# Kernel tuning notes

Measured on AMD Instinct MI355X. Metric: run time of the kernel, lower is better.

Reference implementation:

```python
import jax, jax.numpy as jnp
import numpy as np

B, S, H, I = 4, 2048, 4096, 11008

def setup_inputs() -> dict:
    key = jax.random.key(0)
    k0, k1, k2, k3 = jax.random.split(key, 4)
    scale = 0.02  # typical init scale for stability
    return {
        "x": jax.random.normal(k0, (B, S, H), dtype=jnp.float32),
        "w_gate": jax.random.normal(k1, (I, H), dtype=jnp.float32) * scale,
        "w_up": jax.random.normal(k2, (I, H), dtype=jnp.float32) * scale,
        "w_down": jax.random.normal(k3, (H, I), dtype=jnp.float32) * scale,
    }

def reference(x, w_gate, w_up, w_down):
    # gate = x @ w_gate^T, up = x @ w_up^T  (torch F.linear convention)
    gate = jnp.einsum("bsh,ih->bsi", x, w_gate)
    up = jnp.einsum("bsh,ih->bsi", x, w_up)
    inter = jax.nn.silu(gate) * up  # SwiGLU
    return jnp.einsum("bsi,hi->bsh", inter, w_down)
```

## Files before the change

### kernel.cpp

```cpp
#include <hip/hip_runtime.h>
#include <hip/hip_bf16.h>
#include <stdint.h>

static constexpr int Hd = 4096;
static constexpr int Id = 11008;
static constexpr int Md = 8192;

using short8 = __attribute__((ext_vector_type(8))) short;
using f32x4  = __attribute__((ext_vector_type(4))) float;

__device__ __forceinline__ unsigned short f2bf(float x) {
    union { float f; unsigned u; } v; v.f = x;
    unsigned r = v.u + 0x7FFF + ((v.u >> 16) & 1);
    return (unsigned short)(r >> 16);
}

typedef const __attribute__((address_space(1))) unsigned int* as1_u32p;
typedef __attribute__((address_space(3))) unsigned int* as3_u32p;

__device__ __forceinline__ void gload16(const unsigned short* g, unsigned short* l) {
    __builtin_amdgcn_global_load_lds((as1_u32p)(const void*)g, (as3_u32p)(void*)l, 16, 0, 0);
}

#define AOFF(r, c) ((((r) * 8) + ((c) ^ ((r) & 7))) * 8)

#define LGKM0() do { asm volatile("s_waitcnt lgkmcnt(0)" ::: "memory"); \
                     __builtin_amdgcn_sched_barrier(0); } while (0)
#define LGKMC8() do { asm volatile("s_waitcnt lgkmcnt(8)" ::: "memory"); } while (0)
#define VMCNT(n) do { asm volatile("s_waitcnt vmcnt(" #n ")" ::: "memory"); \
                      __builtin_amdgcn_sched_barrier(0); } while (0)
#define BARRIER() do { asm volatile("" ::: "memory"); __builtin_amdgcn_s_barrier(); \
                       asm volatile("" ::: "memory"); } while (0)

__global__ __launch_bounds__(256) void k_cvt4(
    const float* __restrict__ s0, unsigned short* __restrict__ d0, int n0,
    const float* __restrict__ s1, unsigned short* __restrict__ d1, int n1,
    const float* __restrict__ s2, unsigned short* __restrict__ d2, int n2,
    const float* __restrict__ s3, unsigned short* __restrict__ d3, int n3)
{
    const int total = n0 + n1 + n2 + n3;
    int i = blockIdx.x * blockDim.x + threadIdx.x;
    const int stride = gridDim.x * blockDim.x;
    for (; i < total; i += stride) {
        const float* s; unsigned short* d; int j = i;
        if (j < n0) { s = s0; d = d0; }
        else { j -= n0;
            if (j < n1) { s = s1; d = d1; }
            else { j -= n1;
                if (j < n2) { s = s2; d = d2; }
                else { j -= n2; s = s3; d = d3; }
            }
        }
        f32x4 a = *(const f32x4*)(s + (size_t)j * 8);
        f32x4 b = *(const f32x4*)(s + (size_t)j * 8 + 4);
        short8 v;
        v[0] = (short)f2bf(a[0]); v[1] = (short)f2bf(a[1]);
        v[2] = (short)f2bf(a[2]); v[3] = (short)f2bf(a[3]);
        v[4] = (short)f2bf(b[0]); v[5] = (short)f2bf(b[1]);
        v[6] = (short)f2bf(b[2]); v[7] = (short)f2bf(b[3]);
        *reinterpret_cast<short8*>(d + (size_t)j * 8) = v;
    }
}

template<int D>
__device__ __forceinline__ void ug_body(
    unsigned short (&As)[2][2][8192], unsigned short (&Gs)[2][8192], unsigned short (&Us)[2][8192],
    const unsigned short* pA0, const unsigned short* pA1,
    const unsigned short* pG0, const unsigned short* pG1,
    const unsigned short* pU0, const unsigned short* pU1,
    int stA, int stGU, bool pfA, bool pfGU,
    int wm, int wn, int r16, int kg, int wave,
    f32x4 (&accg)[8][2], f32x4 (&accu)[8][2])
{
    constexpr size_t hK = (size_t)128 * Hd;
    short8 af[4][2], gf[2][2], uf[2][2];

    if (pfA) {
        gload16(pA0 + stA, &As[D ^ 1][0][wave * 512]);
        gload16(pA1 + stA, &As[D ^ 1][0][4096 + wave * 512]);
    }
    #pragma unroll
    for (int mi = 0; mi < 4; ++mi)
        #pragma unroll
        for (int kk = 0; kk < 2; ++kk)
            af[mi][kk] = *(const short8*)&As[D][wm][AOFF(mi * 16 + r16, kk * 4 + kg)];
    #pragma unroll
    for (int ni = 0; ni < 2; ++ni)
        #pragma unroll
        for (int kk = 0; kk < 2; ++kk)
            gf[ni][kk] = *(const short8*)&Gs[D][AOFF(wn * 32 + ni * 16 + r16, kk * 4 + kg)];
    LGKMC8();
    BARRIER();
    LGKM0();
    __builtin_amdgcn_s_setprio(1);
    #pragma unroll
    for (int mi = 0; mi < 4; ++mi)
        #pragma unroll
        for (int ni = 0; ni < 2; ++ni)
            #pragma unroll
            for (int kk = 0; kk < 2; ++kk)
                accg[mi][ni] = __builtin_amdgcn_mfma_f32_16x16x32_bf16(af[mi][kk], gf[ni][kk], accg[mi][ni], 0, 0, 0);
    __builtin_amdgcn_s_setprio(0);
    BARRIER();

    if (pfA) {
        gload16(pA0 + hK + stA, &As[D ^ 1][1][wave * 512]);
        gload16(pA1 + hK + stA, &As[D ^ 1][1][4096 + wave * 512]);
    }
    #pragma unroll
    for (int ni = 0; ni < 2; ++ni)
        #pragma unroll
        for (int kk = 0; kk < 2; ++kk)
            uf[ni][kk] = *(const short8*)&Us[D][AOFF(wn * 32 + ni * 16 + r16, kk * 4 + kg)];
    BARRIER();
    LGKM0();
    __builtin_amdgcn_s_setprio(1);
    #pragma unroll
    for (int mi = 0; mi < 4; ++mi)
        #pragma unroll
        for (int ni = 0; ni < 2; ++ni)
            #pragma unroll
            for (int kk = 0; kk < 2; ++kk)
                accu[mi][ni] = __builtin_amdgcn_mfma_f32_16x16x32_bf16(af[mi][kk], uf[ni][kk], accu[mi][ni], 0, 0, 0);
    __builtin_amdgcn_s_setprio(0);
    BARRIER();

    if (pfGU) {
        gload16(pG0 + stGU, &Gs[D][wave * 512]);
        gload16(pG1 + stGU, &Gs[D][4096 + wave * 512]);
    }
    #pragma unroll
    for (int mi = 0; mi < 4; ++mi)
        #pragma unroll
        for (int kk = 0; kk < 2; ++kk)
            af[mi][kk] = *(const short8*)&As[D][wm][AOFF((mi + 4) * 16 + r16, kk * 4 + kg)];
    BARRIER();
    LGKM0();
    __builtin_amdgcn_s_setprio(1);
    #pragma unroll
    for (int mi = 0; mi < 4; ++mi)
        #pragma unroll
        for (int ni = 0; ni < 2; ++ni)
            #pragma unroll
            for (int kk = 0; kk < 2; ++kk)
                accg[mi + 4][ni] = __builtin_amdgcn_mfma_f32_16x16x32_bf16(af[mi][kk], gf[ni][kk], accg[mi + 4][ni], 0, 0, 0);
    __builtin_amdgcn_s_setprio(0);
    BARRIER();

    if (pfGU) {
        gload16(pU0 + stGU, &Us[D][wave * 512]);
        gload16(pU1 + stGU, &Us[D][4096 + wave * 512]);
    }
    __builtin_amdgcn_s_setprio(1);
    #pragma unroll
    for (int mi = 0; mi < 4; ++mi)
        #pragma unroll
        for (int ni = 0; ni < 2; ++ni)
            #pragma unroll
            for (int kk = 0; kk < 2; ++kk)
                accu[mi + 4][ni] = __builtin_amdgcn_mfma_f32_16x16x32_bf16(af[mi][kk], uf[ni][kk], accu[mi + 4][ni], 0, 0, 0);
    __builtin_amdgcn_s_setprio(0);
    if (pfGU) { VMCNT(4); }
    else      { VMCNT(0); }
    BARRIER();
}

__global__ __launch_bounds__(512, 2) void k_upgate(
    const unsigned short* __restrict__ A,
    const unsigned short* __restrict__ G,
    const unsigned short* __restrict__ U,
    unsigned short* __restrict__ inter)
{
    __shared__ unsigned short As[2][2][8192];
    __shared__ unsigned short Gs[2][8192];
    __shared__ unsigned short Us[2][8192];

    const int tid  = threadIdx.x;
    const int wave = tid >> 6;
    const int lane = tid & 63;
    const int wm   = wave >> 2;
    const int wn   = wave & 3;
    const int r16  = lane & 15;
    const int kg   = lane >> 4;

    const int nwg = gridDim.x;
    const int bid = blockIdx.x;
    const int swz = (bid & 7) * (nwg >> 3) + (bid >> 3);
    const int grp = swz / 688;
    const int rem = swz % 688;
    const int m0  = (grp * 8 + (rem & 7)) * 256;
    const int n0  = (rem >> 3) * 128;

    const int i0 = tid,       r0 = i0 >> 3;
    const int i1 = 512 + tid, r1 = i1 >> 3;
    const int cc0 = (i0 & 7) ^ (r0 & 7);
    const int cc1 = (i1 & 7) ^ (r1 & 7);
    constexpr size_t hK = (size_t)128 * Hd;

    const unsigned short* pA0 = A + (size_t)(m0 + r0) * Hd + cc0 * 8;
    const unsigned short* pA1 = A + (size_t)(m0 + r1) * Hd + cc1 * 8;
    const unsigned short* pG0 = G + (size_t)(n0 + r0) * Hd + cc0 * 8;
    const unsigned short* pG1 = G + (size_t)(n0 + r1) * Hd + cc1 * 8;
    const unsigned short* pU0 = U + (size_t)(n0 + r0) * Hd + cc0 * 8;
    const unsigned short* pU1 = U + (size_t)(n0 + r1) * Hd + cc1 * 8;

    f32x4 accg[8][2] = {};
    f32x4 accu[8][2] = {};

    constexpr int NT = Hd >> 6;

    gload16(pA0,      &As[0][0][wave * 512]);
    gload16(pA1,      &As[0][0][4096 + wave * 512]);
    gload16(pA0 + hK, &As[0][1][wave * 512]);
    gload16(pA1 + hK, &As[0][1][4096 + wave * 512]);
    gload16(pG0,      &Gs[0][wave * 512]);
    gload16(pG1,      &Gs[0][4096 + wave * 512]);
    gload16(pU0,      &Us[0][wave * 512]);
    gload16(pU1,      &Us[0][4096 + wave * 512]);
    gload16(pG0 + 64, &Gs[1][wave * 512]);
    gload16(pG1 + 64, &Gs[1][4096 + wave * 512]);
    gload16(pU0 + 64, &Us[1][wave * 512]);
    gload16(pU1 + 64, &Us[1][4096 + wave * 512]);
    VMCNT(4);
    BARRIER();

    for (int kt = 0; kt < NT; kt += 2) {
        ug_body<0>(As, Gs, Us, pA0, pA1, pG0, pG1, pU0, pU1,
                   64, 128, true, (kt + 2) < NT, wm, wn, r16, kg, wave, accg, accu);
        ug_body<1>(As, Gs, Us, pA0, pA1, pG0, pG1, pU0, pU1,
                   128, 192, (kt + 2) < NT, (kt + 3) < NT, wm, wn, r16, kg, wave, accg, accu);
        pA0 += 128; pA1 += 128; pG0 += 128; pG1 += 128; pU0 += 128; pU1 += 128;
    }

    #pragma unroll
    for (int mi = 0; mi < 8; ++mi)
        #pragma unroll
        for (int ni = 0; ni < 2; ++ni) {
            const int row = m0 + wm * 128 + mi * 16 + kg * 4;
            const int col = n0 + wn * 32 + ni * 16 + r16;
            f32x4 g = accg[mi][ni], u = accu[mi][ni];
            #pragma unroll
            for (int rr = 0; rr < 4; ++rr) {
                float gv = g[rr];
                float s  = gv / (1.0f + __expf(-gv));
                inter[(size_t)(row + rr) * Id + col] = f2bf(s * u[rr]);
            }
        }
}

template<int D>
__device__ __forceinline__ void ktile_body(
    unsigned short (&As)[2][2][8192], unsigned short (&Bs)[2][2][8192],
    const unsigned short* pA0, const unsigned short* pA1,
    const unsigned short* pB0, const unsigned short* pB1,
    size_t hK, int stA, int stB, bool pfA, bool pfB,
    int wm, int wn, int r16, int kg, int wave,
    f32x4 (&acc)[8][4], short8 (&af)[4][2], short8 (&b0f)[2][2], short8 (&b1f)[2][2])
{
    if (pfA) {
        gload16(pA0 + stA, &As[D ^ 1][0][wave * 512]);
        gload16(pA1 + stA, &As[D ^ 1][0][4096 + wave * 512]);
    }
    #pragma unroll
    for (int mi = 0; mi < 4; ++mi)
        #pragma unroll
        for (int kk = 0; kk < 2; ++kk)
            af[mi][kk] = *(const short8*)&As[D][wm][AOFF(mi * 16 + r16, kk * 4 + kg)];
    #pragma unroll
    for (int ni = 0; ni < 2; ++ni)
        #pragma unroll
        for (int kk = 0; kk < 2; ++kk)
            b0f[ni][kk] = *(const short8*)&Bs[D][wn >> 1][AOFF((wn & 1) * 64 + ni * 16 + r16, kk * 4 + kg)];
    LGKMC8();
    BARRIER();
    LGKM0();
    __builtin_amdgcn_s_setprio(1);
    #pragma unroll
    for (int mi = 0; mi < 4; ++mi)
        #pragma unroll
        for (int ni = 0; ni < 2; ++ni)
            #pragma unroll
            for (int kk = 0; kk < 2; ++kk)
                acc[mi][ni] = __builtin_amdgcn_mfma_f32_16x16x32_bf16(af[mi][kk], b0f[ni][kk], acc[mi][ni], 0, 0, 0);
    __builtin_amdgcn_s_setprio(0);
    BARRIER();

    if (pfA) {
        gload16(pA0 + hK + stA, &As[D ^ 1][1][wave * 512]);
        gload16(pA1 + hK + stA, &As[D ^ 1][1][4096 + wave * 512]);
    }
    #pragma unroll
    for (int ni = 0; ni < 2; ++ni)
        #pragma unroll
        for (int kk = 0; kk < 2; ++kk)
            b1f[ni][kk] = *(const short8*)&Bs[D][wn >> 1][AOFF((wn & 1) * 64 + (ni + 2) * 16 + r16, kk * 4 + kg)];
    BARRIER();
    LGKM0();
    __builtin_amdgcn_s_setprio(1);
    #pragma unroll
    for (int mi = 0; mi < 4; ++mi)
        #pragma unroll
        for (int ni = 0; ni < 2; ++ni)
            #pragma unroll
            for (int kk = 0; kk < 2; ++kk)
                acc[mi][ni + 2] = __builtin_amdgcn_mfma_f32_16x16x32_bf16(af[mi][kk], b1f[ni][kk], acc[mi][ni + 2], 0, 0, 0);
    __builtin_amdgcn_s_setprio(0);
    BARRIER();

    if (pfB) {
        gload16(pB0 + stB, &Bs[D][0][wave * 512]);
        gload16(pB1 + stB, &Bs[D][0][4096 + wave * 512]);
    }
    #pragma unroll
    for (int mi = 0; mi < 4; ++mi)
        #pragma unroll
        for (int kk = 0; kk < 2; ++kk)
            af[mi][kk] = *(const short8*)&As[D][wm][AOFF((mi + 4) * 16 + r16, kk * 4 + kg)];
    BARRIER();
    LGKM0();
    __builtin_amdgcn_s_setprio(1);
    #pragma unroll
    for (int mi = 0; mi < 4; ++mi)
        #pragma unroll
        for (int ni = 0; ni < 2; ++ni)
            #pragma unroll
            for (int kk = 0; kk < 2; ++kk)
                acc[mi + 4][ni + 2] = __builtin_amdgcn_mfma_f32_16x16x32_bf16(af[mi][kk], b1f[ni][kk], acc[mi + 4][ni + 2], 0, 0, 0);
    __builtin_amdgcn_s_setprio(0);
    BARRIER();

    if (pfB) {
        gload16(pB0 + hK + stB, &Bs[D][1][wave * 512]);
        gload16(pB1 + hK + stB, &Bs[D][1][4096 + wave * 512]);
    }
    __builtin_amdgcn_s_setprio(1);
    #pragma unroll
    for (int mi = 0; mi < 4; ++mi)
        #pragma unroll
        for (int ni = 0; ni < 2; ++ni)
            #pragma unroll
            for (int kk = 0; kk < 2; ++kk)
                acc[mi + 4][ni] = __builtin_amdgcn_mfma_f32_16x16x32_bf16(af[mi][kk], b0f[ni][kk], acc[mi + 4][ni], 0, 0, 0);
    __builtin_amdgcn_s_setprio(0);
    if (pfB) { VMCNT(4); }
    else     { VMCNT(0); }
    BARRIER();
}

__global__ __launch_bounds__(512, 2) void k_down(
    const unsigned short* __restrict__ A, const unsigned short* __restrict__ B,
    float* __restrict__ Cf, const int K, const int ldC)
{
    __shared__ unsigned short As[2][2][8192];
    __shared__ unsigned short Bs[2][2][8192];

    const int tid  = threadIdx.x;
    const int wave = tid >> 6;
    const int lane = tid & 63;
    const int wm   = wave >> 2;
    const int wn   = wave & 3;
    const int r16  = lane & 15;
    const int kg   = lane >> 4;

    const int nwg = gridDim.x;
    const int bid = blockIdx.x;
    const int swz = (bid & 7) * (nwg >> 3) + (bid >> 3);
    const int grp = swz / 128;
    const int rem = swz % 128;
    const int m0  = (grp * 8 + (rem & 7)) * 256;
    const int n0  = (rem >> 3) * 256;

    const int i0 = tid,       r0 = i0 >> 3;
    const int i1 = 512 + tid, r1 = i1 >> 3;
    const int cc0 = (i0 & 7) ^ (r0 & 7);
    const int cc1 = (i1 & 7) ^ (r1 & 7);
    const size_t hK = (size_t)128 * K;

    const unsigned short* pA0 = A + (size_t)(m0 + r0) * K + cc0 * 8;
    const unsigned short* pA1 = A + (size_t)(m0 + r1) * K + cc1 * 8;
    const unsigned short* pB0 = B + (size_t)(n0 + r0) * K + cc0 * 8;
    const unsigned short* pB1 = B + (size_t)(n0 + r1) * K + cc1 * 8;

    f32x4 acc[8][4] = {};
    short8 af[4][2], b0f[2][2], b1f[2][2];

    const int NT = K >> 6;

    gload16(pA0,      &As[0][0][wave * 512]);
    gload16(pA1,      &As[0][0][4096 + wave * 512]);
    gload16(pA0 + hK, &As[0][1][wave * 512]);
    gload16(pA1 + hK, &As[0][1][4096 + wave * 512]);
    gload16(pB0,      &Bs[0][0][wave * 512]);
    gload16(pB1,      &Bs[0][0][4096 + wave * 512]);
    gload16(pB0 + hK, &Bs[0][1][wave * 512]);
    gload16(pB1 + hK, &Bs[0][1][4096 + wave * 512]);
    gload16(pB0 + 64,      &Bs[1][0][wave * 512]);
    gload16(pB1 + 64,      &Bs[1][0][4096 + wave * 512]);
    gload16(pB0 + hK + 64, &Bs[1][1][wave * 512]);
    gload16(pB1 + hK + 64, &Bs[1][1][4096 + wave * 512]);
    VMCNT(4);
    BARRIER();

    for (int kt = 0; kt < NT; kt += 2) {
        ktile_body<0>(As, Bs, pA0, pA1, pB0, pB1, hK, 64, 128,
                      true, (kt + 2) < NT, wm, wn, r16, kg, wave, acc, af, b0f, b1f);
        ktile_body<1>(As, Bs, pA0, pA1, pB0, pB1, hK, 128, 192,
                      (kt + 2) < NT, (kt + 3) < NT, wm, wn, r16, kg, wave, acc, af, b0f, b1f);
        pA0 += 128; pA1 += 128; pB0 += 128; pB1 += 128;
    }

    #pragma unroll
    for (int mi = 0; mi < 8; ++mi)
        #pragma unroll
        for (int ni = 0; ni < 4; ++ni) {
            const int row = m0 + wm * 128 + mi * 16 + kg * 4;
            const int col = n0 + wn * 64 + ni * 16 + r16;
            f32x4 v = acc[mi][ni];
            #pragma unroll
            for (int rr = 0; rr < 4; ++rr)
                Cf[(size_t)(row + rr) * ldC + col] = v[rr];
        }
}

extern "C" void kernel_launch(void* const* d_in, const int* in_sizes, int n_in,
                              void* d_out, int out_size, void* d_ws, size_t ws_size,
                              hipStream_t stream) {
    const float* x  = (const float*)d_in[0];
    const float* wg = (const float*)d_in[1];
    const float* wu = (const float*)d_in[2];
    const float* wd = (const float*)d_in[3];
    float* out = (float*)d_out;

    unsigned short* inter = (unsigned short*)d_ws;
    unsigned short* xb  = (unsigned short*)((char*)d_ws + (size_t)Md * Id * 2);
    unsigned short* wgb = xb  + (size_t)Md * Hd;
    unsigned short* wub = wgb + (size_t)Id * Hd;
    unsigned short* wdb = wub + (size_t)Id * Hd;

    k_cvt4<<<dim3(2048), dim3(256), 0, stream>>>(
        x,  xb,  Md * Hd / 8,
        wg, wgb, Id * Hd / 8,
        wu, wub, Id * Hd / 8,
        wd, wdb, Id * Hd / 8);

    k_upgate<<<dim3((Md / 256) * (Id / 128)), dim3(512), 0, stream>>>(xb, wgb, wub, inter);
    k_down<<<dim3((Md / 256) * (Hd / 256)), dim3(512), 0, stream>>>(inter, wdb, out, Id, Hd);
}
```

Before: 2.338 ms.

## Collapse four-phase k-tile pipeline into two phases with fewer barriers

Restructures the per-k-tile body of both the up/gate and down GEMM kernels. It goes from four barrier-separated compute phases to two. All A-tile prefetches are issued together, all LDS fragments are loaded up front, and the explicit lgkmcnt waits and intermediate barriers are removed. Fragment registers move into the body function, and the prefetch predicates are corrected so the last tile is not loaded past the end. This reduces barrier stalls per k-step, at the cost of higher register pressure and less interleaving of global loads with MFMA.

Result: faster. 2.048 ms (-12.4%).

```diff
diff --git a/kernel.cpp b/kernel.cpp
--- a/kernel.cpp
+++ b/kernel.cpp
@@ -24,9 +24,6 @@
 
 #define AOFF(r, c) ((((r) * 8) + ((c) ^ ((r) & 7))) * 8)
 
-#define LGKM0() do { asm volatile("s_waitcnt lgkmcnt(0)" ::: "memory"); \
-                     __builtin_amdgcn_sched_barrier(0); } while (0)
-#define LGKMC8() do { asm volatile("s_waitcnt lgkmcnt(8)" ::: "memory"); } while (0)
 #define VMCNT(n) do { asm volatile("s_waitcnt vmcnt(" #n ")" ::: "memory"); \
                       __builtin_amdgcn_sched_barrier(0); } while (0)
 #define BARRIER() do { asm volatile("" ::: "memory"); __builtin_amdgcn_s_barrier(); \
@@ -76,45 +73,34 @@
     short8 af[4][2], gf[2][2], uf[2][2];
 
     if (pfA) {
-        gload16(pA0 + stA, &As[D ^ 1][0][wave * 512]);
-        gload16(pA1 + stA, &As[D ^ 1][0][4096 + wave * 512]);
-    }
-    #pragma unroll
-    for (int mi = 0; mi < 4; ++mi)
-        #pragma unroll
-        for (int kk = 0; kk < 2; ++kk)
-            af[mi][kk] = *(const short8*)&As[D][wm][AOFF(mi * 16 + r16, kk * 4 + kg)];
-    #pragma unroll
-    for (int ni = 0; ni < 2; ++ni)
-        #pragma unroll
-        for (int kk = 0; kk < 2; ++kk)
-            gf[ni][kk] = *(const short8*)&Gs[D][AOFF(wn * 32 + ni * 16 + r16, kk * 4 + kg)];
-    LGKMC8();
-    BARRIER();
-    LGKM0();
-    __builtin_amdgcn_s_setprio(1);
-    #pragma unroll
-    for (int mi = 0; mi < 4; ++mi)
-        #pragma unroll
-        for (int ni = 0; ni < 2; ++ni)
-            #pragma unroll
-            for (int kk = 0; kk < 2; ++kk)
-                accg[mi][ni] = __builtin_amdgcn_mfma_f32_16x16x32_bf16(af[mi][kk], gf[ni][kk], accg[mi][ni], 0, 0, 0);
-    __builtin_amdgcn_s_setprio(0);
-    BARRIER();
-
-    if (pfA) {
+        gload16(pA0 + stA,      &As[D ^ 1][0][wave * 512]);
+        gload16(pA1 + stA,      &As[D ^ 1][0][4096 + wave * 512]);
         gload16(pA0 + hK + stA, &As[D ^ 1][1][wave * 512]);
         gload16(pA1 + hK + stA, &As[D ^ 1][1][4096 + wave * 512]);
     }
     #pragma unroll
+    for (int mi = 0; mi < 4; ++mi)
+        #pragma unroll
+        for (int kk = 0; kk < 2; ++kk)
+            af[mi][kk] = *(const short8*)&As[D][wm][AOFF(mi * 16 + r16, kk * 4 + kg)];
+    #pragma unroll
     for (int ni = 0; ni < 2; ++ni)
         #pragma unroll
         for (int kk = 0; kk < 2; ++kk)
+            gf[ni][kk] = *(const short8*)&Gs[D][AOFF(wn * 32 + ni * 16 + r16, kk * 4 + kg)];
+    #pragma unroll
+    for (int ni = 0; ni < 2; ++ni)
+        #pragma unroll
+        for (int kk = 0; kk < 2; ++kk)
             uf[ni][kk] = *(const short8*)&Us[D][AOFF(wn * 32 + ni * 16 + r16, kk * 4 + kg)];
-    BARRIER();
-    LGKM0();
     __builtin_amdgcn_s_setprio(1);
+    #pragma unroll
+    for (int mi = 0; mi < 4; ++mi)
+        #pragma unroll
+        for (int ni = 0; ni < 2; ++ni)
+            #pragma unroll
+            for (int kk = 0; kk < 2; ++kk)
+                accg[mi][ni] = __builtin_amdgcn_mfma_f32_16x16x32_bf16(af[mi][kk], gf[ni][kk], accg[mi][ni], 0, 0, 0);
     #pragma unroll
     for (int mi = 0; mi < 4; ++mi)
         #pragma unroll
@@ -128,30 +114,22 @@
     if (pfGU) {
         gload16(pG0 + stGU, &Gs[D][wave * 512]);
         gload16(pG1 + stGU, &Gs[D][4096 + wave * 512]);
-    }
-    #pragma unroll
-    for (int mi = 0; mi < 4; ++mi)
-        #pragma unroll
-        for (int kk = 0; kk < 2; ++kk)
-            af[mi][kk] = *(const short8*)&As[D][wm][AOFF((mi + 4) * 16 + r16, kk * 4 + kg)];
-    BARRIER();
-    LGKM0();
-    __builtin_amdgcn_s_setprio(1);
-    #pragma unroll
-    for (int mi = 0; mi < 4; ++mi)
-        #pragma unroll
-        for (int ni = 0; ni < 2; ++ni)
-            #pragma unroll
-            for (int kk = 0; kk < 2; ++kk)
-                accg[mi + 4][ni] = __builtin_amdgcn_mfma_f32_16x16x32_bf16(af[mi][kk], gf[ni][kk], accg[mi + 4][ni], 0, 0, 0);
-    __builtin_amdgcn_s_setprio(0);
-    BARRIER();
-
-    if (pfGU) {
         gload16(pU0 + stGU, &Us[D][wave * 512]);
         gload16(pU1 + stGU, &Us[D][4096 + wave * 512]);
     }
+    #pragma unroll
+    for (int mi = 0; mi < 4; ++mi)
+        #pragma unroll
+        for (int kk = 0; kk < 2; ++kk)
+            af[mi][kk] = *(const short8*)&As[D][wm][AOFF((mi + 4) * 16 + r16, kk * 4 + kg)];
     __builtin_amdgcn_s_setprio(1);
+    #pragma unroll
+    for (int mi = 0; mi < 4; ++mi)
+        #pragma unroll
+        for (int ni = 0; ni < 2; ++ni)
+            #pragma unroll
+            for (int kk = 0; kk < 2; ++kk)
+                accg[mi + 4][ni] = __builtin_amdgcn_mfma_f32_16x16x32_bf16(af[mi][kk], gf[ni][kk], accg[mi + 4][ni], 0, 0, 0);
     #pragma unroll
     for (int mi = 0; mi < 4; ++mi)
         #pragma unroll
@@ -225,10 +203,13 @@
     BARRIER();
 
     for (int kt = 0; kt < NT; kt += 2) {
+        const bool p1 = (kt + 1) < NT;
+        const bool p2 = (kt + 2) < NT;
+        const bool p3 = (kt + 3) < NT;
         ug_body<0>(As, Gs, Us, pA0, pA1, pG0, pG1, pU0, pU1,
-                   64, 128, true, (kt + 2) < NT, wm, wn, r16, kg, wave, accg, accu);
+                   64, 128, p1, p2, wm, wn, r16, kg, wave, accg, accu);
         ug_body<1>(As, Gs, Us, pA0, pA1, pG0, pG1, pU0, pU1,
-                   128, 192, (kt + 2) < NT, (kt + 3) < NT, wm, wn, r16, kg, wave, accg, accu);
+                   128, 192, p2, p3, wm, wn, r16, kg, wave, accg, accu);
         pA0 += 128; pA1 += 128; pG0 += 128; pG1 += 128; pU0 += 128; pU1 += 128;
     }
 
@@ -255,48 +236,39 @@
     const unsigned short* pB0, const unsigned short* pB1,
     size_t hK, int stA, int stB, bool pfA, bool pfB,
     int wm, int wn, int r16, int kg, int wave,
-    f32x4 (&acc)[8][4], short8 (&af)[4][2], short8 (&b0f)[2][2], short8 (&b1f)[2][2])
+    f32x4 (&acc)[8][4])
 {
+    short8 af[4][2], b0f[2][2], b1f[2][2];
+
     if (pfA) {
-        gload16(pA0 + stA, &As[D ^ 1][0][wave * 512]);
-        gload16(pA1 + stA, &As[D ^ 1][0][4096 + wave * 512]);
-    }
-    #pragma unroll
-    for (int mi = 0; mi < 4; ++mi)
-        #pragma unroll
-        for (int kk = 0; kk < 2; ++kk)
-            af[mi][kk] = *(const short8*)&As[D][wm][AOFF(mi * 16 + r16, kk * 4 + kg)];
-    #pragma unroll
-    for (int ni = 0; ni < 2; ++ni)
-        #pragma unroll
-        for (int kk = 0; kk < 2; ++kk)
-            b0f[ni][kk] = *(const short8*)&Bs[D][wn >> 1][AOFF((wn & 1) * 64 + ni * 16 + r16, kk * 4 + kg)];
-    LGKMC8();
-    BARRIER();
-    LGKM0();
-    __builtin_amdgcn_s_setprio(1);
-    #pragma unroll
-    for (int mi = 0; mi < 4; ++mi)
-        #pragma unroll
-        for (int ni = 0; ni < 2; ++ni)
-            #pragma unroll
-            for (int kk = 0; kk < 2; ++kk)
-                acc[mi][ni] = __builtin_amdgcn_mfma_f32_16x16x32_bf16(af[mi][kk], b0f[ni][kk], acc[mi][ni], 0, 0, 0);
-    __builtin_amdgcn_s_setprio(0);
-    BARRIER();
-
-    if (pfA) {
+        gload16(pA0 + stA,      &As[D ^ 1][0][wave * 512]);
+        gload16(pA1 + stA,      &As[D ^ 1][0][4096 + wave * 512]);
         gload16(pA0 + hK + stA, &As[D ^ 1][1][wave * 512]);
         gload16(pA1 + hK + stA, &As[D ^ 1][1][4096 + wave * 512]);
     }
     #pragma unroll
+    for (int mi = 0; mi < 4; ++mi)
+        #pragma unroll
+        for (int kk = 0; kk < 2; ++kk)
+            af[mi][kk] = *(const short8*)&As[D][wm][AOFF(mi * 16 + r16, kk * 4 + kg)];
+    #pragma unroll
     for (int ni = 0; ni < 2; ++ni)
         #pragma unroll
         for (int kk = 0; kk < 2; ++kk)
+            b0f[ni][kk] = *(const short8*)&Bs[D][wn >> 1][AOFF((wn & 1) * 64 + ni * 16 + r16, kk * 4 + kg)];
+    #pragma unroll
+    for (int ni = 0; ni < 2; ++ni)
+        #pragma unroll
+        for (int kk = 0; kk < 2; ++kk)
             b1f[ni][kk] = *(const short8*)&Bs[D][wn >> 1][AOFF((wn & 1) * 64 + (ni + 2) * 16 + r16, kk * 4 + kg)];
-    BARRIER();
-    LGKM0();
     __builtin_amdgcn_s_setprio(1);
+    #pragma unroll
+    for (int mi = 0; mi < 4; ++mi)
+        #pragma unroll
+        for (int ni = 0; ni < 2; ++ni)
+            #pragma unroll
+            for (int kk = 0; kk < 2; ++kk)
+                acc[mi][ni] = __builtin_amdgcn_mfma_f32_16x16x32_bf16(af[mi][kk], b0f[ni][kk], acc[mi][ni], 0, 0, 0);
     #pragma unroll
     for (int mi = 0; mi < 4; ++mi)
         #pragma unroll
@@ -308,32 +280,24 @@
     BARRIER();
 
     if (pfB) {
-        gload16(pB0 + stB, &Bs[D][0][wave * 512]);
-        gload16(pB1 + stB, &Bs[D][0][4096 + wave * 512]);
-    }
-    #pragma unroll
-    for (int mi = 0; mi < 4; ++mi)
-        #pragma unroll
-        for (int kk = 0; kk < 2; ++kk)
-            af[mi][kk] = *(const short8*)&As[D][wm][AOFF((mi + 4) * 16 + r16, kk * 4 + kg)];
-    BARRIER();
-    LGKM0();
-    __builtin_amdgcn_s_setprio(1);
-    #pragma unroll
-    for (int mi = 0; mi < 4; ++mi)
-        #pragma unroll
-        for (int ni = 0; ni < 2; ++ni)
-            #pragma unroll
-            for (int kk = 0; kk < 2; ++kk)
-                acc[mi + 4][ni + 2] = __builtin_amdgcn_mfma_f32_16x16x32_bf16(af[mi][kk], b1f[ni][kk], acc[mi + 4][ni + 2], 0, 0, 0);
-    __builtin_amdgcn_s_setprio(0);
-    BARRIER();
-
-    if (pfB) {
+        gload16(pB0 + stB,      &Bs[D][0][wave * 512]);
+        gload16(pB1 + stB,      &Bs[D][0][4096 + wave * 512]);
         gload16(pB0 + hK + stB, &Bs[D][1][wave * 512]);
         gload16(pB1 + hK + stB, &Bs[D][1][4096 + wave * 512]);
     }
+    #pragma unroll
+    for (int mi = 0; mi < 4; ++mi)
+        #pragma unroll
+        for (int kk = 0; kk < 2; ++kk)
+            af[mi][kk] = *(const short8*)&As[D][wm][AOFF((mi + 4) * 16 + r16, kk * 4 + kg)];
     __builtin_amdgcn_s_setprio(1);
+    #pragma unroll
+    for (int mi = 0; mi < 4; ++mi)
+        #pragma unroll
+        for (int ni = 0; ni < 2; ++ni)
+            #pragma unroll
+            for (int kk = 0; kk < 2; ++kk)
+                acc[mi + 4][ni + 2] = __builtin_amdgcn_mfma_f32_16x16x32_bf16(af[mi][kk], b1f[ni][kk], acc[mi + 4][ni + 2], 0, 0, 0);
     #pragma unroll
     for (int mi = 0; mi < 4; ++mi)
         #pragma unroll
@@ -382,7 +346,6 @@
     const unsigned short* pB1 = B + (size_t)(n0 + r1) * K + cc1 * 8;
 
     f32x4 acc[8][4] = {};
-    short8 af[4][2], b0f[2][2], b1f[2][2];
 
     const int NT = K >> 6;
 
@@ -402,10 +365,13 @@
     BARRIER();
 
     for (int kt = 0; kt < NT; kt += 2) {
-        ktile_body<0>(As, Bs, pA0, pA1, pB0, pB1, hK, 64, 128,
-                      true, (kt + 2) < NT, wm, wn, r16, kg, wave, acc, af, b0f, b1f);
-        ktile_body<1>(As, Bs, pA0, pA1, pB0, pB1, hK, 128, 192,
-                      (kt + 2) < NT, (kt + 3) < NT, wm, wn, r16, kg, wave, acc, af, b0f, b1f);
+        const bool p1 = (kt + 1) < NT;
+        const bool p2 = (kt + 2) < NT;
+        const bool p3 = (kt + 3) < NT;
+        ktile_body<0>(As, Bs, pA0, pA1, pB0, pB1, hK, 64, 128, p1, p2,
+                      wm, wn, r16, kg, wave, acc);
+        ktile_body<1>(As, Bs, pA0, pA1, pB0, pB1, hK, 128, 192, p2, p3,
+                      wm, wn, r16, kg, wave, acc);
         pA0 += 128; pA1 += 128; pB0 += 128; pB1 += 128;
     }
 
```
